# Kernel optimization log

Hardware: AMD Instinct MI355X
Metric: run time of the kernel (lower is better)

## Reference

```python
import jax, jax.numpy as jnp
import numpy as np

TAU = 2.0      # LIF membrane time constant (spikingjelly default-style, decay_input=True)
VTH = 0.5      # v_threshold from init
S = 4          # time_steps
EPS = 1e-5     # BatchNorm eps
ALPHA = 4.0    # surrogate sigmoid alpha (spikingjelly Sigmoid default)

@jax.custom_vjp
def spike(x):
    # Heaviside forward (spikingjelly: x >= 0 -> 1)
    return (x >= 0.0).astype(x.dtype)

def _spike_fwd(x):
    return spike(x), x

def _spike_bwd(x, g):
    sg = jax.nn.sigmoid(ALPHA * x)
    return (g * ALPHA * sg * (1.0 - sg),)

spike.defvjp(_spike_fwd, _spike_bwd)

def bn(y, gamma, beta, mean, var):
    # inference-mode BatchNorm2d over channel axis 1; y: (B, C, T, V)
    inv = gamma * jax.lax.rsqrt(var + EPS)
    return y * inv[None, :, None, None] + (beta - mean * inv)[None, :, None, None]


def setup_inputs() -> dict:
    key = jax.random.key(0)
    ks = jax.random.split(key, 16)
    B, T, C, V, H, NC = 16, 512, 3, 16, 128, 12
    inp = {
        "x": jax.random.normal(ks[0], (B, T, C, V), dtype=jnp.float32),
        "w1": jax.random.normal(ks[1], (H, C), dtype=jnp.float32) * (1.0 / np.sqrt(C)),
        "b1": jax.random.normal(ks[2], (H,), dtype=jnp.float32) * 0.01,
        "g1": jnp.ones((H,), jnp.float32),
        "be1": jnp.zeros((H,), jnp.float32),
        "m1": jax.random.normal(ks[3], (H,), dtype=jnp.float32) * 0.1,
        "rv1": jax.random.uniform(ks[4], (H,), dtype=jnp.float32) + 0.5,
        "w2": jax.random.normal(ks[5], (H, H), dtype=jnp.float32) * (1.0 / np.sqrt(H)),
        "b2": jax.random.normal(ks[6], (H,), dtype=jnp.float32) * 0.01,
        "g2": jnp.ones((H,), jnp.float32),
        "be2": jnp.zeros((H,), jnp.float32),
        "m2": jax.random.normal(ks[7], (H,), dtype=jnp.float32) * 0.1,
        "rv2": jax.random.uniform(ks[8], (H,), dtype=jnp.float32) + 0.5,
        "wc": jax.random.normal(ks[9], (NC, H), dtype=jnp.float32) * (1.0 / np.sqrt(H)),
        "bc": jax.random.normal(ks[10], (NC,), dtype=jnp.float32) * 0.01,
    }
    return inp


def reference(x, w1, b1, g1, be1, m1, rv1, w2, b2, g2, be2, m2, rv2, wc, bc):
    # x: (B, T, C, V) -> channels-first (B, C, T, V) as in torch permute
    xc = jnp.transpose(x, (0, 2, 1, 3))
    # fc1 1x1 conv + BN; input identical across all S steps, so compute once
    h1 = bn(jnp.einsum('bctv,oc->botv', xc, w1) + b1[None, :, None, None],
            g1, be1, m1, rv1)  # (B, H, T, V)

    def step(carry, _):
        v1s, v2s, acc = carry
        # LIF1: decay_input=True, v_reset=0 hard reset
        v1n = v1s + (h1 - v1s) / TAU
        s1 = spike(v1n - VTH)
        v1n = v1n * (1.0 - s1)
        # fc2 1x1 conv + BN on spikes
        h2 = bn(jnp.einsum('botv,po->bptv', s1, w2) + b2[None, :, None, None],
                g2, be2, m2, rv2)
        # LIF2
        v2n = v2s + (h2 - v2s) / TAU
        s2 = spike(v2n - VTH)
        v2n = v2n * (1.0 - s2)
        return (v1n, v2n, acc + s2), None

    z = jnp.zeros_like(h1)
    (_, _, acc), _ = jax.lax.scan(step, (z, z, z), None, length=S)
    # mean over S, then mean over T and V -> (B, H); dropout is identity in eval
    feat = (acc / S).mean(axis=(2, 3))
    return feat @ wc.T + bc
```

## Files before the change

kernel.cpp:

```cpp
#include <hip/hip_runtime.h>
#include <hip/hip_bf16.h>
#include <stdint.h>
#include <math.h>

#define B_ 16
#define T_ 512
#define V_ 16
#define H_ 128
#define NC_ 12

typedef float v2f __attribute__((ext_vector_type(2)));
typedef __attribute__((ext_vector_type(8))) short s8frag;
typedef __attribute__((ext_vector_type(4))) float f4frag;
typedef unsigned long long u64;


__global__ __launch_bounds__(256) void zero_feat_kernel(float* __restrict__ feat) {
    int i = blockIdx.x * 256 + threadIdx.x;
    if (i < B_ * H_) feat[i] = 0.f;
}

__device__ __forceinline__ unsigned short bf16_rne(float w) {
    unsigned u = __float_as_uint(w);
    unsigned r = (u + 0x7FFFu + ((u >> 16) & 1u)) >> 16;
    return (unsigned short)r;
}
__device__ __forceinline__ float bf16_f32(unsigned short h) {
    return __uint_as_float((unsigned)h << 16);
}
__device__ __forceinline__ void split8(const float* __restrict__ s, s8frag& hi, s8frag& lo) {
    #pragma unroll
    for (int j = 0; j < 8; ++j) {
        float w = s[j];
        unsigned short hb = bf16_rne(w);
        unsigned short lb = bf16_rne(w - bf16_f32(hb));
        hi[j] = (short)hb;
        lo[j] = (short)lb;
    }
}

__device__ __forceinline__ uint4 expand8(unsigned bt) {
    uint4 r;
    r.x = ((bt      & 1u) * 0x3F80u) | (((bt >> 1) & 1u) * 0x3F800000u);
    r.y = (((bt >> 2) & 1u) * 0x3F80u) | (((bt >> 3) & 1u) * 0x3F800000u);
    r.z = (((bt >> 4) & 1u) * 0x3F80u) | (((bt >> 5) & 1u) * 0x3F800000u);
    r.w = (((bt >> 6) & 1u) * 0x3F80u) | (((bt >> 7) & 1u) * 0x3F800000u);
    return r;
}

#define ROUNDS 8
__global__ __launch_bounds__(256, 4) void snn_main(
    const float* __restrict__ x,
    const float* __restrict__ w1, const float* __restrict__ b1,
    const float* __restrict__ g1, const float* __restrict__ be1,
    const float* __restrict__ m1, const float* __restrict__ rv1,
    const float* __restrict__ w2, const float* __restrict__ b2,
    const float* __restrict__ g2, const float* __restrict__ be2,
    const float* __restrict__ m2, const float* __restrict__ rv2,
    float* __restrict__ feat)
{
    __shared__ uint4 afrag[2][4][4][64];
    __shared__ uint4 msk[4][16];

    const int tid  = threadIdx.x;
    const int lane = tid & 63;
    const int wv   = tid >> 6;
    const int kg   = lane >> 4;
    const int nl   = lane & 15;
    const int bb   = blockIdx.x >> 6;
    const int sbase = (blockIdx.x & 63) * (ROUNDS * 16);

    const int p = lane, q = lane + 64;
    v2f w0v = { w1[p*3+0], w1[q*3+0] };
    v2f w1v = { w1[p*3+1], w1[q*3+1] };
    v2f w2v = { w1[p*3+2], w1[q*3+2] };
    v2f b1v = { b1[p], b1[q] };
    float i1a = g1[p] * (float)(1.0 / sqrt((double)(rv1[p] + 1e-5f)));
    float i1b = g1[q] * (float)(1.0 / sqrt((double)(rv1[q] + 1e-5f)));
    v2f i1v = { i1a, i1b };
    v2f d1v = { be1[p] - m1[p] * i1a, be1[q] - m1[q] * i1b };

    const int ch0 = wv * 32 + nl;
    const int ch1 = ch0 + 16;
    float i2c0 = g2[ch0] * (float)(1.0 / sqrt((double)(rv2[ch0] + 1e-5f)));
    float d2c0 = be2[ch0] - m2[ch0] * i2c0;
    float b2c0 = b2[ch0];
    float i2c1 = g2[ch1] * (float)(1.0 / sqrt((double)(rv2[ch1] + 1e-5f)));
    float d2c1 = be2[ch1] - m2[ch1] * i2c1;
    float b2c1 = b2[ch1];

    s8frag bh0[4], bl0[4], bh1[4], bl1[4];
    #pragma unroll
    for (int c = 0; c < 4; ++c) {
        split8(&w2[ch0 * H_ + c * 32 + kg * 8], bh0[c], bl0[c]);
        split8(&w2[ch1 * H_ + c * 32 + kg * 8], bh1[c], bl1[c]);
    }

    float facc0 = 0.f, facc1 = 0.f;

    #define CONSUME(BUF)                                                        \
        for (int tt = 0; tt < 4; ++tt) {                                        \
            s8frag a0 = *(const s8frag*)&afrag[BUF][tt][0][lane];               \
            s8frag a1 = *(const s8frag*)&afrag[BUF][tt][1][lane];               \
            s8frag a2 = *(const s8frag*)&afrag[BUF][tt][2][lane];               \
            s8frag a3 = *(const s8frag*)&afrag[BUF][tt][3][lane];               \
            f4frag acc0 = {0.f,0.f,0.f,0.f}, acc1 = {0.f,0.f,0.f,0.f};          \
            acc0 = __builtin_amdgcn_mfma_f32_16x16x32_bf16(a0, bh0[0], acc0, 0,0,0); \
            acc0 = __builtin_amdgcn_mfma_f32_16x16x32_bf16(a1, bh0[1], acc0, 0,0,0); \
            acc0 = __builtin_amdgcn_mfma_f32_16x16x32_bf16(a2, bh0[2], acc0, 0,0,0); \
            acc0 = __builtin_amdgcn_mfma_f32_16x16x32_bf16(a3, bh0[3], acc0, 0,0,0); \
            acc0 = __builtin_amdgcn_mfma_f32_16x16x32_bf16(a0, bl0[0], acc0, 0,0,0); \
            acc0 = __builtin_amdgcn_mfma_f32_16x16x32_bf16(a1, bl0[1], acc0, 0,0,0); \
            acc0 = __builtin_amdgcn_mfma_f32_16x16x32_bf16(a2, bl0[2], acc0, 0,0,0); \
            acc0 = __builtin_amdgcn_mfma_f32_16x16x32_bf16(a3, bl0[3], acc0, 0,0,0); \
            acc1 = __builtin_amdgcn_mfma_f32_16x16x32_bf16(a0, bh1[0], acc1, 0,0,0); \
            acc1 = __builtin_amdgcn_mfma_f32_16x16x32_bf16(a1, bh1[1], acc1, 0,0,0); \
            acc1 = __builtin_amdgcn_mfma_f32_16x16x32_bf16(a2, bh1[2], acc1, 0,0,0); \
            acc1 = __builtin_amdgcn_mfma_f32_16x16x32_bf16(a3, bh1[3], acc1, 0,0,0); \
            acc1 = __builtin_amdgcn_mfma_f32_16x16x32_bf16(a0, bl1[0], acc1, 0,0,0); \
            acc1 = __builtin_amdgcn_mfma_f32_16x16x32_bf16(a1, bl1[1], acc1, 0,0,0); \
            acc1 = __builtin_amdgcn_mfma_f32_16x16x32_bf16(a2, bl1[2], acc1, 0,0,0); \
            acc1 = __builtin_amdgcn_mfma_f32_16x16x32_bf16(a3, bl1[3], acc1, 0,0,0); \
            float v0 = 0.f, v1 = 0.f;                                           \
            _Pragma("unroll")                                                   \
            for (int s = 0; s < 4; ++s) {                                       \
                float h20 = (acc0[s] + b2c0) * i2c0 + d2c0;                     \
                float h21 = (acc1[s] + b2c1) * i2c1 + d2c1;                     \
                v0 = v0 + (h20 - v0) * 0.5f;                                    \
                v1 = v1 + (h21 - v1) * 0.5f;                                    \
                bool s0 = v0 >= 0.5f, s1 = v1 >= 0.5f;                          \
                v0 = s0 ? 0.f : v0;  v1 = s1 ? 0.f : v1;                        \
                facc0 += s0 ? 1.f : 0.f;  facc1 += s1 ? 1.f : 0.f;              \
            }                                                                   \
        }

    for (int r = 0; r < ROUNDS; ++r) {
        #pragma unroll
        for (int i = 0; i < 4; ++i) {
            int site = sbase + r * 16 + wv * 4 + i;
            int t = site >> 4, v = site & 15;
            const float* xp = x + ((size_t)(bb * T_ + t) * 3) * V_ + v;
            float x0 = xp[0], x1 = xp[V_], x2 = xp[2 * V_];

            v2f h1 = ((x0 * w0v + x1 * w1v + x2 * w2v) + b1v) * i1v + d1v;
            v2f v1t = h1 * 0.5f;
            v2f v2t = v1t + h1 * 0.25f;
            v2f v3t = v2t + (h1 - v2t) * 0.5f;
            v2f v4t = v3t + (h1 - v3t) * 0.5f;

            u64 t1a = __ballot(v1t.x >= 0.5f), t2a = __ballot(v2t.x >= 0.5f);
            u64 t3a = __ballot(v3t.x >= 0.5f), t4a = __ballot(v4t.x >= 0.5f);
            u64 t1b = __ballot(v1t.y >= 0.5f), t2b = __ballot(v2t.y >= 0.5f);
            u64 t3b = __ballot(v3t.y >= 0.5f), t4b = __ballot(v4t.y >= 0.5f);
            u64 s3a = t1a | (t3a & ~t2a), s3b = t1b | (t3b & ~t2b);
            u64 s4a = t2a | (t4a & ~t3a), s4b = t2b | (t4b & ~t3b);

            u64 mx = (lane == 0) ? t1a : (lane == 1) ? t2a : (lane == 2) ? s3a : s4a;
            u64 my = (lane == 0) ? t1b : (lane == 1) ? t2b : (lane == 2) ? s3b : s4b;
            if (lane < 4) {
                uint4 mm;
                mm.x = (unsigned)mx; mm.y = (unsigned)(mx >> 32);
                mm.z = (unsigned)my; mm.w = (unsigned)(my >> 32);
                msk[wv][i * 4 + lane] = mm;
            }
        }
        {
            uint4 mm = msk[wv][nl];
            u64 wx = (u64)mm.x | ((u64)mm.y << 32);
            u64 wy = (u64)mm.z | ((u64)mm.w << 32);
            int sh = kg << 3;
            int buf = r & 1;
            afrag[buf][wv][0][lane] = expand8((unsigned)(wx >> sh) & 0xFFu);
            afrag[buf][wv][1][lane] = expand8((unsigned)(wx >> (sh + 32)) & 0xFFu);
            afrag[buf][wv][2][lane] = expand8((unsigned)(wy >> sh) & 0xFFu);
            afrag[buf][wv][3][lane] = expand8((unsigned)(wy >> (sh + 32)) & 0xFFu);
        }
        if (r > 0) { int pb = (r - 1) & 1; CONSUME(pb); }
        __syncthreads();
    }
    { int pb = (ROUNDS - 1) & 1; CONSUME(pb); }
    #undef CONSUME

    facc0 += __shfl_xor(facc0, 16); facc0 += __shfl_xor(facc0, 32);
    facc1 += __shfl_xor(facc1, 16); facc1 += __shfl_xor(facc1, 32);
    if (lane < 16) {
        atomicAdd(&feat[bb * H_ + ch0], facc0);
        atomicAdd(&feat[bb * H_ + ch1], facc1);
    }
}

__global__ __launch_bounds__(128) void classifier_kernel(
    const float* __restrict__ feat,
    const float* __restrict__ wc,
    const float* __restrict__ bc,
    float* __restrict__ out) {
    __shared__ float fb[H_];
    int b = blockIdx.x, t = threadIdx.x;
    fb[t] = feat[b * H_ + t] * (1.0f / 32768.0f);
    __syncthreads();
    if (t < NC_) {
        float s = 0.f;
        for (int h = 0; h < H_; ++h) s += fb[h] * wc[t * H_ + h];
        out[b * NC_ + t] = s + bc[t];
    }
}

extern "C" void kernel_launch(void* const* d_in, const int* in_sizes, int n_in,
                              void* d_out, int out_size, void* d_ws, size_t ws_size,
                              hipStream_t stream) {
    const float* x   = (const float*)d_in[0];
    const float* w1  = (const float*)d_in[1];
    const float* b1  = (const float*)d_in[2];
    const float* g1  = (const float*)d_in[3];
    const float* be1 = (const float*)d_in[4];
    const float* m1  = (const float*)d_in[5];
    const float* rv1 = (const float*)d_in[6];
    const float* w2  = (const float*)d_in[7];
    const float* b2  = (const float*)d_in[8];
    const float* g2  = (const float*)d_in[9];
    const float* be2 = (const float*)d_in[10];
    const float* m2  = (const float*)d_in[11];
    const float* rv2 = (const float*)d_in[12];
    const float* wc  = (const float*)d_in[13];
    const float* bc  = (const float*)d_in[14];

    float* feat = (float*)d_ws;
    float* out  = (float*)d_out;

    zero_feat_kernel<<<8, 256, 0, stream>>>(feat);
    snn_main<<<1024, 256, 0, stream>>>(x, w1, b1, g1, be1, m1, rv1,
                                       w2, b2, g2, be2, m2, rv2, feat);
    classifier_kernel<<<B_, 128, 0, stream>>>(feat, wc, bc, out);
}
```

Measured before the change: 151.7 us.

## Fuse classifier into main kernel via last-block completion counter; split MFMA chains

```diff
diff --git a/kernel.cpp b/kernel.cpp
--- a/kernel.cpp
+++ b/kernel.cpp
@@ -14,10 +14,10 @@
 typedef __attribute__((ext_vector_type(4))) float f4frag;
 typedef unsigned long long u64;
 
-
-__global__ __launch_bounds__(256) void zero_feat_kernel(float* __restrict__ feat) {
-    int i = blockIdx.x * 256 + threadIdx.x;
-    if (i < B_ * H_) feat[i] = 0.f;
+#define WS_DONE 2048
+
+__global__ __launch_bounds__(1024) void zero_ws_kernel(float* __restrict__ ws) {
+    for (int i = threadIdx.x; i < B_ * H_ + 4; i += 1024) ws[i] = 0.f;
 }
 
 __device__ __forceinline__ unsigned short bf16_rne(float w) {
@@ -57,10 +57,13 @@
     const float* __restrict__ w2, const float* __restrict__ b2,
     const float* __restrict__ g2, const float* __restrict__ be2,
     const float* __restrict__ m2, const float* __restrict__ rv2,
-    float* __restrict__ feat)
+    const float* __restrict__ wc, const float* __restrict__ bc,
+    float* __restrict__ feat, float* __restrict__ done,
+    float* __restrict__ out)
 {
     __shared__ uint4 afrag[2][4][4][64];
     __shared__ uint4 msk[4][16];
+    __shared__ float lastf;
 
     const int tid  = threadIdx.x;
     const int lane = tid & 63;
@@ -104,23 +107,25 @@
             s8frag a1 = *(const s8frag*)&afrag[BUF][tt][1][lane];               \
             s8frag a2 = *(const s8frag*)&afrag[BUF][tt][2][lane];               \
             s8frag a3 = *(const s8frag*)&afrag[BUF][tt][3][lane];               \
-            f4frag acc0 = {0.f,0.f,0.f,0.f}, acc1 = {0.f,0.f,0.f,0.f};          \
-            acc0 = __builtin_amdgcn_mfma_f32_16x16x32_bf16(a0, bh0[0], acc0, 0,0,0); \
-            acc0 = __builtin_amdgcn_mfma_f32_16x16x32_bf16(a1, bh0[1], acc0, 0,0,0); \
-            acc0 = __builtin_amdgcn_mfma_f32_16x16x32_bf16(a2, bh0[2], acc0, 0,0,0); \
-            acc0 = __builtin_amdgcn_mfma_f32_16x16x32_bf16(a3, bh0[3], acc0, 0,0,0); \
-            acc0 = __builtin_amdgcn_mfma_f32_16x16x32_bf16(a0, bl0[0], acc0, 0,0,0); \
-            acc0 = __builtin_amdgcn_mfma_f32_16x16x32_bf16(a1, bl0[1], acc0, 0,0,0); \
-            acc0 = __builtin_amdgcn_mfma_f32_16x16x32_bf16(a2, bl0[2], acc0, 0,0,0); \
-            acc0 = __builtin_amdgcn_mfma_f32_16x16x32_bf16(a3, bl0[3], acc0, 0,0,0); \
-            acc1 = __builtin_amdgcn_mfma_f32_16x16x32_bf16(a0, bh1[0], acc1, 0,0,0); \
-            acc1 = __builtin_amdgcn_mfma_f32_16x16x32_bf16(a1, bh1[1], acc1, 0,0,0); \
-            acc1 = __builtin_amdgcn_mfma_f32_16x16x32_bf16(a2, bh1[2], acc1, 0,0,0); \
-            acc1 = __builtin_amdgcn_mfma_f32_16x16x32_bf16(a3, bh1[3], acc1, 0,0,0); \
-            acc1 = __builtin_amdgcn_mfma_f32_16x16x32_bf16(a0, bl1[0], acc1, 0,0,0); \
-            acc1 = __builtin_amdgcn_mfma_f32_16x16x32_bf16(a1, bl1[1], acc1, 0,0,0); \
-            acc1 = __builtin_amdgcn_mfma_f32_16x16x32_bf16(a2, bl1[2], acc1, 0,0,0); \
-            acc1 = __builtin_amdgcn_mfma_f32_16x16x32_bf16(a3, bl1[3], acc1, 0,0,0); \
+            f4frag a0h = {0.f,0.f,0.f,0.f}, a0l = {0.f,0.f,0.f,0.f};            \
+            f4frag a1h = {0.f,0.f,0.f,0.f}, a1l = {0.f,0.f,0.f,0.f};            \
+            a0h = __builtin_amdgcn_mfma_f32_16x16x32_bf16(a0, bh0[0], a0h, 0,0,0); \
+            a0l = __builtin_amdgcn_mfma_f32_16x16x32_bf16(a0, bl0[0], a0l, 0,0,0); \
+            a1h = __builtin_amdgcn_mfma_f32_16x16x32_bf16(a0, bh1[0], a1h, 0,0,0); \
+            a1l = __builtin_amdgcn_mfma_f32_16x16x32_bf16(a0, bl1[0], a1l, 0,0,0); \
+            a0h = __builtin_amdgcn_mfma_f32_16x16x32_bf16(a1, bh0[1], a0h, 0,0,0); \
+            a0l = __builtin_amdgcn_mfma_f32_16x16x32_bf16(a1, bl0[1], a0l, 0,0,0); \
+            a1h = __builtin_amdgcn_mfma_f32_16x16x32_bf16(a1, bh1[1], a1h, 0,0,0); \
+            a1l = __builtin_amdgcn_mfma_f32_16x16x32_bf16(a1, bl1[1], a1l, 0,0,0); \
+            a0h = __builtin_amdgcn_mfma_f32_16x16x32_bf16(a2, bh0[2], a0h, 0,0,0); \
+            a0l = __builtin_amdgcn_mfma_f32_16x16x32_bf16(a2, bl0[2], a0l, 0,0,0); \
+            a1h = __builtin_amdgcn_mfma_f32_16x16x32_bf16(a2, bh1[2], a1h, 0,0,0); \
+            a1l = __builtin_amdgcn_mfma_f32_16x16x32_bf16(a2, bl1[2], a1l, 0,0,0); \
+            a0h = __builtin_amdgcn_mfma_f32_16x16x32_bf16(a3, bh0[3], a0h, 0,0,0); \
+            a0l = __builtin_amdgcn_mfma_f32_16x16x32_bf16(a3, bl0[3], a0l, 0,0,0); \
+            a1h = __builtin_amdgcn_mfma_f32_16x16x32_bf16(a3, bh1[3], a1h, 0,0,0); \
+            a1l = __builtin_amdgcn_mfma_f32_16x16x32_bf16(a3, bl1[3], a1l, 0,0,0); \
+            f4frag acc0 = a0h + a0l, acc1 = a1h + a1l;                          \
             float v0 = 0.f, v1 = 0.f;                                           \
             _Pragma("unroll")                                                   \
             for (int s = 0; s < 4; ++s) {                                       \
@@ -187,21 +192,26 @@
         atomicAdd(&feat[bb * H_ + ch0], facc0);
         atomicAdd(&feat[bb * H_ + ch1], facc1);
     }
-}
-
-__global__ __launch_bounds__(128) void classifier_kernel(
-    const float* __restrict__ feat,
-    const float* __restrict__ wc,
-    const float* __restrict__ bc,
-    float* __restrict__ out) {
-    __shared__ float fb[H_];
-    int b = blockIdx.x, t = threadIdx.x;
-    fb[t] = feat[b * H_ + t] * (1.0f / 32768.0f);
+
+    __threadfence();
     __syncthreads();
-    if (t < NC_) {
-        float s = 0.f;
-        for (int h = 0; h < H_; ++h) s += fb[h] * wc[t * H_ + h];
-        out[b * NC_ + t] = s + bc[t];
+    if (tid == 0) lastf = atomicAdd(done, 1.0f);
+    __syncthreads();
+    if (lastf >= 1022.5f) {
+        float* fb  = (float*)afrag;
+        float* wcb = fb + B_ * H_;
+        for (int i = tid; i < B_ * H_; i += 256)
+            fb[i] = atomicAdd(&feat[i], 0.0f) * (1.0f / 32768.0f);
+        for (int i = tid; i < NC_ * H_; i += 256)
+            wcb[i] = wc[i];
+        __syncthreads();
+        if (tid < B_ * NC_) {
+            int b = tid / NC_, n = tid % NC_;
+            float s = 0.f;
+            #pragma unroll 8
+            for (int h = 0; h < H_; ++h) s += fb[b * H_ + h] * wcb[n * H_ + h];
+            out[tid] = s + bc[n];
+        }
     }
 }
 
@@ -224,11 +234,13 @@
     const float* wc  = (const float*)d_in[13];
     const float* bc  = (const float*)d_in[14];
 
-    float* feat = (float*)d_ws;
+    float* ws   = (float*)d_ws;
+    float* feat = ws;
+    float* done = ws + WS_DONE;
     float* out  = (float*)d_out;
 
-    zero_feat_kernel<<<8, 256, 0, stream>>>(feat);
+    zero_ws_kernel<<<1, 1024, 0, stream>>>(ws);
     snn_main<<<1024, 256, 0, stream>>>(x, w1, b1, g1, be1, m1, rv1,
-                                       w2, b2, g2, be2, m2, rv2, feat);
-    classifier_kernel<<<B_, 128, 0, stream>>>(feat, wc, bc, out);
-}
+                                       w2, b2, g2, be2, m2, rv2,
+                                       wc, bc, feat, done, out);
+}
```

Measured after the change: 260.9 us. 1.72x slower.
